# Performance work log

Measured on AMD Instinct MI355X. Metric: run time of the kernel, lower is better.

## Reference

```python
import jax, jax.numpy as jnp
import numpy as np

OUT, IN = 4096, 4096          # weight_shape
T, K, GROUP = 256, 2, 256     # trellis window, bits/weight, weight_scales_group_size
GRID = np.array([-3.0, -1.0, 1.0, 3.0], dtype=np.float32) / np.sqrt(5.0)  # 2-bit symmetric, unit-power


def fwht(x):
    """Normalized fast Walsh-Hadamard transform along the last axis (H = H^T, orthonormal)."""
    n = x.shape[-1]
    orig = x.shape
    y = x.reshape(-1, n)
    rows = y.shape[0]
    h = 1
    while h < n:
        y = y.reshape(rows, n // (2 * h), 2, h)
        a, b = y[:, :, 0, :], y[:, :, 1, :]
        y = jnp.stack([a + b, a - b], axis=2)
        h *= 2
    return y.reshape(orig) * (1.0 / np.sqrt(n)).astype(np.float32)


def fake_quant_u8_per_channel(x):
    """InputQuantizer: 8-bit PER_CHANNEL asymmetric fake-quant over the last (in-channel) dim."""
    red = tuple(range(x.ndim - 1))
    xmin = jnp.min(x, axis=red)
    xmax = jnp.max(x, axis=red)
    scale = jnp.maximum((xmax - xmin) / 255.0, 1e-8)
    zero = jnp.round(-xmin / scale)
    q = jnp.clip(jnp.round(x / scale) + zero, 0.0, 255.0)
    dq = (q - zero) * scale
    # straight-through estimator (matches torch fake-quant training behavior)
    return x + jax.lax.stop_gradient(dq - x)


def decode_trellis(trellis):
    """LowBitSym decode: unpack K=2-bit codes from packed 16-bit trellis words and map
    to the symmetric unit-power 2-bit grid. trellis: (NV, T//16*K) int -> (OUT, IN) float."""
    shifts = jnp.arange(14, -1, -2, dtype=jnp.int32)         # MSB-first 2-bit fields
    codes = (trellis[:, :, None] >> shifts) & 3               # (NV, 32, 8)
    grid = jnp.asarray(GRID)
    return grid[codes].reshape(OUT, IN)


def setup_inputs() -> dict:
    key = jax.random.key(0)
    k1, k2, k3, k4, k5 = jax.random.split(key, 5)
    x = jax.random.normal(k1, (4, 2048, IN), dtype=jnp.float32)
    SU = jax.random.normal(k2, (IN,), dtype=jnp.float32)
    SV = jax.random.normal(k3, (OUT,), dtype=jnp.float32)
    weight_scales = jax.random.uniform(k4, (OUT * IN // GROUP, 1), dtype=jnp.float32)
    trellis = jax.random.randint(k5, (OUT * IN // T, T // 16 * K), 0, 65536, dtype=jnp.int32)
    return {"x": x, "SU": SU, "SV": SV, "weight_scales": weight_scales, "trellis": trellis}


def reference(x, SU, SV, weight_scales, trellis):
    # activation path: incoherence rotate + 8-bit fake quant
    xh = fwht(x * SU)                       # matmul_hadUt_cuda(x * SU)
    xq = fake_quant_u8_per_channel(xh)
    # weight path: trellis decode + Hadamard + SV + grouped scales
    w = decode_trellis(trellis)             # (OUT, IN)
    w = (fwht(w.T) * SV).T                  # (matmul_hadU_cuda(w.T) * SV).T
    w = (w.reshape(-1, GROUP) * weight_scales).reshape(OUT, IN)
    # F.linear(input=xq, weight=w)
    return jnp.einsum('bsi,oi->bso', xq, w)
```

## Files before the change

### kernel.cpp

```cpp
#include <hip/hip_runtime.h>
#include <hip/hip_bf16.h>
#include <stdint.h>

#define IN_DIM 4096
#define OUT_DIM 4096
#define M_ROWS 8192

typedef __attribute__((ext_vector_type(8))) short s16x8;
typedef __attribute__((ext_vector_type(4))) float f32x4;

__device__ __forceinline__ unsigned short f2bf(float f) {
  uint32_t u = __float_as_uint(f);
  uint32_t r = (u + 0x7fffu + ((u >> 16) & 1u)) >> 16;
  return (unsigned short)r;
}
__device__ __forceinline__ float b2f(unsigned short u) {
  return __uint_as_float((uint32_t)u << 16);
}

__device__ __forceinline__ void async16(void* lds, const void* g) {
  __builtin_amdgcn_global_load_lds(
      (const __attribute__((address_space(1))) unsigned int*)g,
      (__attribute__((address_space(3))) unsigned int*)lds, 16, 0, 0);
}

#define FENCE asm volatile("" ::: "memory")

__device__ __forceinline__ void h16(float (&v)[16]) {
#pragma unroll
  for (int h = 1; h < 16; h <<= 1) {
#pragma unroll
    for (int g = 0; g < 8; ++g) {
      int r = g & (h - 1);
      int i0 = ((g & ~(h - 1)) << 1) | r;
      float a = v[i0], b = v[i0 + h];
      v[i0] = a + b;
      v[i0 + h] = a - b;
    }
  }
}

__global__ void fwht_x_kernel(const float* __restrict__ x, const float* __restrict__ SU,
                              unsigned short* __restrict__ xh) {
  __shared__ float s[4352];
  const int row = blockIdx.x;
  const int t = threadIdx.x;
  float v[16];
  const float* xr = x + (size_t)row * IN_DIM;
#pragma unroll
  for (int a = 0; a < 16; ++a) {
    int i = a * 256 + t;
    v[a] = xr[i] * SU[i];
  }
  h16(v);
#pragma unroll
  for (int a = 0; a < 16; ++a) {
    int i = a * 256 + t;
    s[i + (i >> 4)] = v[a];
  }
  __syncthreads();
  const int A = t >> 4, C = t & 15;
#pragma unroll
  for (int b = 0; b < 16; ++b) {
    int i = A * 256 + b * 16 + C;
    v[b] = s[i + (i >> 4)];
  }
  h16(v);
  __syncthreads();
#pragma unroll
  for (int b = 0; b < 16; ++b) {
    int i = A * 256 + b * 16 + C;
    s[i + (i >> 4)] = v[b];
  }
  __syncthreads();
#pragma unroll
  for (int c = 0; c < 16; ++c) {
    int i = t * 16 + c;
    v[c] = s[i + (i >> 4)];
  }
  h16(v);
  unsigned short ob[16];
#pragma unroll
  for (int c = 0; c < 16; ++c) ob[c] = f2bf(v[c] * 0.015625f);
  s16x8* dst = (s16x8*)(xh + (size_t)row * IN_DIM + t * 16);
  dst[0] = *(s16x8*)&ob[0];
  dst[1] = *(s16x8*)&ob[8];
}

__global__ void minmax_part_kernel(const unsigned short* __restrict__ xh,
                                   float* __restrict__ pmin, float* __restrict__ pmax) {
  const int rc = blockIdx.x >> 3;
  const int cb = blockIdx.x & 7;
  const int ch0 = cb * 512 + threadIdx.x * 2;
  float mn0 = 3.4e38f, mx0 = -3.4e38f, mn1 = 3.4e38f, mx1 = -3.4e38f;
  const unsigned int* base =
      (const unsigned int*)(xh + (size_t)rc * 256 * IN_DIM + ch0);
  for (int r = 0; r < 256; ++r) {
    unsigned int u = base[(size_t)r * (IN_DIM / 2)];
    float v0 = __uint_as_float(u << 16);
    float v1 = __uint_as_float(u & 0xffff0000u);
    mn0 = fminf(mn0, v0); mx0 = fmaxf(mx0, v0);
    mn1 = fminf(mn1, v1); mx1 = fmaxf(mx1, v1);
  }
  pmin[rc * IN_DIM + ch0] = mn0;
  pmin[rc * IN_DIM + ch0 + 1] = mn1;
  pmax[rc * IN_DIM + ch0] = mx0;
  pmax[rc * IN_DIM + ch0 + 1] = mx1;
}

__global__ void minmax_fin_kernel(const float* __restrict__ pmin, const float* __restrict__ pmax,
                                  float* __restrict__ scale, float* __restrict__ zero) {
  int ch = blockIdx.x * 256 + threadIdx.x;
  float mn = 3.4e38f, mx = -3.4e38f;
  for (int rc = 0; rc < 32; ++rc) {
    mn = fminf(mn, pmin[rc * IN_DIM + ch]);
    mx = fmaxf(mx, pmax[rc * IN_DIM + ch]);
  }
  float sc = fmaxf((mx - mn) / 255.0f, 1e-8f);
  float zp = rintf(-mn / sc);
  scale[ch] = sc;
  zero[ch] = zp;
}

__global__ void quant_kernel(const unsigned short* __restrict__ xh,
                             const float* __restrict__ scale, const float* __restrict__ zero,
                             unsigned short* __restrict__ xq) {
  const int total8 = M_ROWS * IN_DIM / 8;
  for (int i8 = blockIdx.x * blockDim.x + threadIdx.x; i8 < total8;
       i8 += gridDim.x * blockDim.x) {
    int c8 = i8 & (IN_DIM / 8 - 1);
    s16x8 v = ((const s16x8*)xh)[i8];
    unsigned short o[8];
#pragma unroll
    for (int j = 0; j < 8; ++j) {
      float sc = scale[c8 * 8 + j];
      float zp = zero[c8 * 8 + j];
      float f = b2f((unsigned short)v[j]);
      float q = fminf(fmaxf(rintf(f / sc) + zp, 0.f), 255.f);
      o[j] = f2bf((q - zp) * sc);
    }
    ((s16x8*)xq)[i8] = *(s16x8*)&o[0];
  }
}

#define W_RADIX4(TARR)                                                     \
  for (int h = 1; h < 64; h <<= 2) {                                       \
    __syncthreads();                                                       \
    _Pragma("unroll") for (int j = 0; j < 4; ++j) {                        \
      int g = j * 256 + tid;                                               \
      int c = g & 63, u = g >> 6;                                          \
      int r = u & (h - 1);                                                 \
      int i0 = ((u & ~(h - 1)) << 2) | r;                                  \
      float a = TARR[i0][c], b2 = TARR[i0 + h][c];                         \
      float c2 = TARR[i0 + 2 * h][c], d = TARR[i0 + 3 * h][c];             \
      float y0 = a + b2, y1 = a - b2, y2 = c2 + d, y3 = c2 - d;            \
      TARR[i0][c] = y0 + y2;                                               \
      TARR[i0 + h][c] = y1 + y3;                                           \
      TARR[i0 + 2 * h][c] = y0 - y2;                                       \
      TARR[i0 + 3 * h][c] = y1 - y3;                                       \
    }                                                                      \
  }                                                                        \
  __syncthreads();

__global__ void fwht_w_inner_fused(const int* __restrict__ trellis,
                                   unsigned short* __restrict__ w) {
  __shared__ float t[64][65];
  const int ohi = blockIdx.x >> 6;
  const int it  = blockIdx.x & 63;
  const int tid = threadIdx.x;
  const float g = 0.44721359549995793f;
#pragma unroll
  for (int j = 0; j < 2; ++j) {
    int wi = j * 256 + tid;
    int r = wi >> 3, wc = wi & 7;
    int word = trellis[(size_t)(ohi * 64 + r) * 512 + it * 8 + wc];
#pragma unroll
    for (int jj = 0; jj < 8; ++jj) {
      int code = (word >> (14 - 2 * jj)) & 3;
      t[r][wc * 8 + jj] = (float)(2 * code - 3) * g;
    }
  }
  W_RADIX4(t)
#pragma unroll
  for (int j = 0; j < 16; ++j) {
    int e = j * 256 + tid;
    int r = e >> 6, c = e & 63;
    w[((size_t)(ohi * 64 + r)) * IN_DIM + it * 64 + c] = f2bf(t[r][c]);
  }
}

__global__ void fwht_w_outer(const unsigned short* __restrict__ w,
                             const float* __restrict__ SV,
                             const float* __restrict__ wscale, unsigned short* __restrict__ wq) {
  __shared__ float t[64][65];
  const int olo = blockIdx.x >> 6;
  const int it  = blockIdx.x & 63;
  const int tid = threadIdx.x;
#pragma unroll
  for (int j = 0; j < 16; ++j) {
    int e = j * 256 + tid;
    int r = e >> 6, c = e & 63;
    t[r][c] = b2f(w[((size_t)(r * 64 + olo)) * IN_DIM + it * 64 + c]);
  }
  W_RADIX4(t)
#pragma unroll
  for (int j = 0; j < 16; ++j) {
    int e = j * 256 + tid;
    int r = e >> 6, c = e & 63;
    int o = r * 64 + olo;
    int i = it * 64 + c;
    float val = t[r][c] * 0.015625f * SV[o] * wscale[(o << 4) + (i >> 8)];
    wq[(size_t)o * IN_DIM + i] = f2bf(val);
  }
}

__global__ __launch_bounds__(512, 2) void gemm256_kernel(
    const unsigned short* __restrict__ A, const unsigned short* __restrict__ B,
    float* __restrict__ C) {
  __shared__ __align__(16) unsigned short lds[65536];
  const int tid  = threadIdx.x;
  const int lane = tid & 63;
  const int wave = tid >> 6;
  const int wm = wave >> 2, wn = wave & 3;
  const int fr = lane & 15, kqi = lane >> 4;
  const int swz = fr & 7;

  const int b  = blockIdx.x;
  const int wg = (b & 7) * 64 + (b >> 3);
  const int bm = wg >> 4, bn = wg & 15;
  const int gm0 = bm * 256, gn0 = bn * 256;

  f32x4 acc[2][2][4][2] = {};
  s16x8 af0[4][2], af1[4][2];
  s16x8 bf0[2][2], bf1[2][2];

  const int F0 = tid, F1 = 512 + tid;
  const int rh0 = F0 >> 3, s0 = (F0 & 7) ^ (rh0 & 7);
  const int rh1 = F1 >> 3, s1 = (F1 & 7) ^ (rh1 & 7);
  auto stage = [&](const unsigned short* gbase, int grow0, int kcol, int ldsoff) {
    async16((void*)&lds[ldsoff + F0 * 8],
            (const void*)(gbase + (size_t)(grow0 + rh0) * IN_DIM + kcol + s0 * 8));
    async16((void*)&lds[ldsoff + F1 * 8],
            (const void*)(gbase + (size_t)(grow0 + rh1) * IN_DIM + kcol + s1 * 8));
  };

#define READ_AF2(DST, QM, TBUF, MIH)                                                      \
  {                                                                                       \
    const int abase = (TBUF) * 16384 + (QM) * 8192;                                       \
    _Pragma("unroll") for (int kk = 0; kk < 2; ++kk)                                      \
      _Pragma("unroll") for (int mi = 2 * (MIH); mi < 2 * (MIH) + 2; ++mi) {              \
        int rh = wm * 64 + mi * 16 + fr;                                                  \
        DST[mi][kk] = *(const s16x8*)&lds[abase + rh * 64 + (((kk * 4 + kqi) ^ swz) * 8)];\
      }                                                                                   \
  }
#define READ_BF2(DST, QN, TBUF, NI)                                                       \
  {                                                                                       \
    const int bbase = 32768 + (TBUF) * 16384 + (QN) * 8192;                               \
    const int rh = wn * 32 + (NI) * 16 + fr;                                              \
    _Pragma("unroll") for (int kk = 0; kk < 2; ++kk)                                      \
      DST[NI][kk] = *(const s16x8*)&lds[bbase + rh * 64 + (((kk * 4 + kqi) ^ swz) * 8)];  \
  }
#define MFMA16(QM, QN, AF, BF)                                                            \
    _Pragma("unroll") for (int kk = 0; kk < 2; ++kk)                                      \
      _Pragma("unroll") for (int mi = 0; mi < 4; ++mi)                                    \
        _Pragma("unroll") for (int ni = 0; ni < 2; ++ni)                                  \
          acc[QM][QN][mi][ni] = __builtin_amdgcn_mfma_f32_16x16x32_bf16(                  \
              AF[mi][kk], BF[ni][kk], acc[QM][QN][mi][ni], 0, 0, 0);
#define PHASE_BEGIN(SGBASE, SGROW0, SKCOL, SLDSOFF, VM)                                   \
    stage(SGBASE, SGROW0, SKCOL, SLDSOFF);                                                \
    FENCE;                                                                                \
    asm volatile("s_waitcnt vmcnt(" #VM ")" ::: "memory");                                \
    __builtin_amdgcn_s_barrier();                                                         \
    FENCE;                                                                                \
    __builtin_amdgcn_s_setprio(1);
#define PHASE_END                                                                         \
    __builtin_amdgcn_s_setprio(0);                                                        \
    FENCE;                                                                                \
    __builtin_amdgcn_s_barrier();                                                         \
    FENCE;

  stage(A, gm0,       0, 0);
  stage(B, gn0,       0, 32768);
  stage(A, gm0 + 128, 0, 8192);
  stage(B, gn0 + 128, 0, 40960);
  stage(A, gm0,      64, 16384);
  stage(B, gn0,      64, 49152);
  FENCE;
  asm volatile("s_waitcnt vmcnt(8)" ::: "memory");
  __builtin_amdgcn_s_barrier();
  FENCE;
  READ_AF2(af0, 0, 0, 0)
  READ_BF2(bf0, 0, 0, 0)

  for (int it = 0; it < 32; ++it) {
    const int k1 = ((2 * it + 1) * 64) & 4095;
    const int k2 = ((2 * it + 2) * 64) & 4095;
    const int k3 = ((2 * it + 3) * 64) & 4095;
    READ_AF2(af0, 0, 0, 1) READ_BF2(bf0, 0, 0, 1)
    PHASE_BEGIN(A, gm0 + 128, k1, 24576, 6)
    MFMA16(0, 0, af0, bf0)
    READ_BF2(bf1, 1, 0, 0) READ_BF2(bf1, 1, 0, 1)
    PHASE_END
    PHASE_BEGIN(B, gn0 + 128, k1, 57344, 63)
    MFMA16(0, 1, af0, bf1)
    READ_AF2(af1, 1, 0, 0)
    PHASE_END
    READ_AF2(af1, 1, 0, 1)
    PHASE_BEGIN(A, gm0,       k2, 0,     63)
    MFMA16(1, 1, af1, bf1)
    PHASE_END
    PHASE_BEGIN(B, gn0,       k2, 32768, 8)
    MFMA16(1, 0, af1, bf0)
    READ_AF2(af0, 0, 1, 0) READ_BF2(bf0, 0, 1, 0)
    PHASE_END
    READ_AF2(af0, 0, 1, 1) READ_BF2(bf0, 0, 1, 1)
    PHASE_BEGIN(A, gm0 + 128, k2, 8192,  6)
    MFMA16(0, 0, af0, bf0)
    READ_BF2(bf1, 1, 1, 0) READ_BF2(bf1, 1, 1, 1)
    PHASE_END
    PHASE_BEGIN(B, gn0 + 128, k2, 40960, 63)
    MFMA16(0, 1, af0, bf1)
    READ_AF2(af1, 1, 1, 0)
    PHASE_END
    READ_AF2(af1, 1, 1, 1)
    PHASE_BEGIN(A, gm0,       k3, 16384, 63)
    MFMA16(1, 1, af1, bf1)
    PHASE_END
    PHASE_BEGIN(B, gn0,       k3, 49152, 8)
    MFMA16(1, 0, af1, bf0)
    READ_AF2(af0, 0, 0, 0) READ_BF2(bf0, 0, 0, 0)
    PHASE_END
  }
#undef PHASE_BEGIN
#undef PHASE_END
#undef MFMA16
#undef READ_AF2
#undef READ_BF2
  asm volatile("s_waitcnt vmcnt(0)" ::: "memory");

  const int orow = kqi * 4;
#pragma unroll
  for (int qm = 0; qm < 2; ++qm)
#pragma unroll
    for (int qn = 0; qn < 2; ++qn)
#pragma unroll
      for (int mi = 0; mi < 4; ++mi)
#pragma unroll
        for (int ni = 0; ni < 2; ++ni) {
          const int row0 = gm0 + qm * 128 + wm * 64 + mi * 16 + orow;
          const int col  = gn0 + qn * 128 + wn * 32 + ni * 16 + fr;
          f32x4 v = acc[qm][qn][mi][ni];
#pragma unroll
          for (int r = 0; r < 4; ++r)
            C[(size_t)(row0 + r) * OUT_DIM + col] = v[r];
        }
}

extern "C" void kernel_launch(void* const* d_in, const int* in_sizes, int n_in,
                              void* d_out, int out_size, void* d_ws, size_t ws_size,
                              hipStream_t stream) {
  const float* x      = (const float*)d_in[0];
  const float* SU     = (const float*)d_in[1];
  const float* SV     = (const float*)d_in[2];
  const float* wscale = (const float*)d_in[3];
  const int* trellis  = (const int*)d_in[4];
  float* out = (float*)d_out;

  char* ws = (char*)d_ws;
  unsigned short* xq = (unsigned short*)ws;
  unsigned short* wq = (unsigned short*)(ws + (size_t)67108864);
  float* pmin  = (float*)(ws + (size_t)67108864);
  float* pmax  = (float*)(ws + (size_t)67108864 + 524288);
  float* scale = (float*)(ws + (size_t)67108864 + 1048576);
  float* zero  = (float*)(ws + (size_t)67108864 + 1064960);

  unsigned short* xh   = (unsigned short*)out;
  unsigned short* wdec = (unsigned short*)out + (size_t)33554432;

  hipLaunchKernelGGL(fwht_x_kernel, dim3(M_ROWS), dim3(256), 0, stream, x, SU, xh);
  hipLaunchKernelGGL(minmax_part_kernel, dim3(256), dim3(256), 0, stream, xh, pmin, pmax);
  hipLaunchKernelGGL(minmax_fin_kernel, dim3(16), dim3(256), 0, stream, pmin, pmax, scale, zero);
  hipLaunchKernelGGL(quant_kernel, dim3(2048), dim3(256), 0, stream, xh, scale, zero, xq);
  hipLaunchKernelGGL(fwht_w_inner_fused, dim3(4096), dim3(256), 0, stream, trellis, wdec);
  hipLaunchKernelGGL(fwht_w_outer, dim3(4096), dim3(256), 0, stream, wdec, SV, wscale, wq);
  hipLaunchKernelGGL(gemm256_kernel, dim3((M_ROWS / 256) * (OUT_DIM / 256)), dim3(512), 0,
                     stream, xq, wq, out);
}
```

Baseline: 336.2 us.

## Fuse weight FWHT into one kernel and merge min/max finalize via atomics

New measurement: 357.6 us. 1.06x slower.

```diff
diff --git a/kernel.cpp b/kernel.cpp
--- a/kernel.cpp
+++ b/kernel.cpp
@@ -16,6 +16,14 @@
 }
 __device__ __forceinline__ float b2f(unsigned short u) {
   return __uint_as_float((uint32_t)u << 16);
+}
+__device__ __forceinline__ unsigned int fmap(float f) {
+  unsigned int u = __float_as_uint(f);
+  return ((int)u >= 0) ? (u | 0x80000000u) : ~u;
+}
+__device__ __forceinline__ float funmap(unsigned int u) {
+  unsigned int b = (u & 0x80000000u) ? (u & 0x7fffffffu) : ~u;
+  return __uint_as_float(b);
 }
 
 __device__ __forceinline__ void async16(void* lds, const void* g) {
@@ -88,7 +96,8 @@
 }
 
 __global__ void minmax_part_kernel(const unsigned short* __restrict__ xh,
-                                   float* __restrict__ pmin, float* __restrict__ pmax) {
+                                   unsigned int* __restrict__ gminU,
+                                   unsigned int* __restrict__ gmaxU) {
   const int rc = blockIdx.x >> 3;
   const int cb = blockIdx.x & 7;
   const int ch0 = cb * 512 + threadIdx.x * 2;
@@ -102,28 +111,15 @@
     mn0 = fminf(mn0, v0); mx0 = fmaxf(mx0, v0);
     mn1 = fminf(mn1, v1); mx1 = fmaxf(mx1, v1);
   }
-  pmin[rc * IN_DIM + ch0] = mn0;
-  pmin[rc * IN_DIM + ch0 + 1] = mn1;
-  pmax[rc * IN_DIM + ch0] = mx0;
-  pmax[rc * IN_DIM + ch0 + 1] = mx1;
-}
-
-__global__ void minmax_fin_kernel(const float* __restrict__ pmin, const float* __restrict__ pmax,
-                                  float* __restrict__ scale, float* __restrict__ zero) {
-  int ch = blockIdx.x * 256 + threadIdx.x;
-  float mn = 3.4e38f, mx = -3.4e38f;
-  for (int rc = 0; rc < 32; ++rc) {
-    mn = fminf(mn, pmin[rc * IN_DIM + ch]);
-    mx = fmaxf(mx, pmax[rc * IN_DIM + ch]);
-  }
-  float sc = fmaxf((mx - mn) / 255.0f, 1e-8f);
-  float zp = rintf(-mn / sc);
-  scale[ch] = sc;
-  zero[ch] = zp;
+  atomicMin(&gminU[ch0], fmap(mn0));
+  atomicMin(&gminU[ch0 + 1], fmap(mn1));
+  atomicMax(&gmaxU[ch0], fmap(mx0));
+  atomicMax(&gmaxU[ch0 + 1], fmap(mx1));
 }
 
 __global__ void quant_kernel(const unsigned short* __restrict__ xh,
-                             const float* __restrict__ scale, const float* __restrict__ zero,
+                             const unsigned int* __restrict__ gminU,
+                             const unsigned int* __restrict__ gmaxU,
                              unsigned short* __restrict__ xq) {
   const int total8 = M_ROWS * IN_DIM / 8;
   for (int i8 = blockIdx.x * blockDim.x + threadIdx.x; i8 < total8;
@@ -133,8 +129,10 @@
     unsigned short o[8];
 #pragma unroll
     for (int j = 0; j < 8; ++j) {
-      float sc = scale[c8 * 8 + j];
-      float zp = zero[c8 * 8 + j];
+      float mn = funmap(gminU[c8 * 8 + j]);
+      float mx = funmap(gmaxU[c8 * 8 + j]);
+      float sc = fmaxf((mx - mn) * (1.0f / 255.0f), 1e-8f);
+      float zp = rintf(-mn / sc);
       float f = b2f((unsigned short)v[j]);
       float q = fminf(fmaxf(rintf(f / sc) + zp, 0.f), 255.f);
       o[j] = f2bf((q - zp) * sc);
@@ -143,74 +141,78 @@
   }
 }
 
-#define W_RADIX4(TARR)                                                     \
-  for (int h = 1; h < 64; h <<= 2) {                                       \
-    __syncthreads();                                                       \
-    _Pragma("unroll") for (int j = 0; j < 4; ++j) {                        \
-      int g = j * 256 + tid;                                               \
-      int c = g & 63, u = g >> 6;                                          \
-      int r = u & (h - 1);                                                 \
-      int i0 = ((u & ~(h - 1)) << 2) | r;                                  \
-      float a = TARR[i0][c], b2 = TARR[i0 + h][c];                         \
-      float c2 = TARR[i0 + 2 * h][c], d = TARR[i0 + 3 * h][c];             \
-      float y0 = a + b2, y1 = a - b2, y2 = c2 + d, y3 = c2 - d;            \
-      TARR[i0][c] = y0 + y2;                                               \
-      TARR[i0 + h][c] = y1 + y3;                                           \
-      TARR[i0 + 2 * h][c] = y0 - y2;                                       \
-      TARR[i0 + 3 * h][c] = y1 - y3;                                       \
-    }                                                                      \
-  }                                                                        \
-  __syncthreads();
-
-__global__ void fwht_w_inner_fused(const int* __restrict__ trellis,
-                                   unsigned short* __restrict__ w) {
-  __shared__ float t[64][65];
-  const int ohi = blockIdx.x >> 6;
-  const int it  = blockIdx.x & 63;
+#define PADA(idx) ((idx) + ((idx) >> 5))
+__global__ __launch_bounds__(1024) void fwht_w_fused(const int* __restrict__ trellis,
+                                                     const float* __restrict__ SV,
+                                                     const float* __restrict__ wscale,
+                                                     unsigned short* __restrict__ wq) {
+  __shared__ float t[16896];
+  const int b = blockIdx.x;
+  const int w = (b & 7) * 128 + (b >> 3);
+  const int ib = w >> 1;
+  const int half = w & 1;
   const int tid = threadIdx.x;
   const float g = 0.44721359549995793f;
-#pragma unroll
-  for (int j = 0; j < 2; ++j) {
-    int wi = j * 256 + tid;
-    int r = wi >> 3, wc = wi & 7;
-    int word = trellis[(size_t)(ohi * 64 + r) * 512 + it * 8 + wc];
-#pragma unroll
-    for (int jj = 0; jj < 8; ++jj) {
-      int code = (word >> (14 - 2 * jj)) & 3;
-      t[r][wc * 8 + jj] = (float)(2 * code - 3) * g;
+
+#pragma unroll
+  for (int j = 0; j < 4; ++j) {
+    int o = j * 1024 + tid;
+    int word = trellis[(size_t)o * 512 + ib];
+#pragma unroll
+    for (int dl = 0; dl < 4; ++dl) {
+      int d = half * 4 + dl;
+      int code = (word >> (14 - 2 * d)) & 3;
+      int idx = dl * 4096 + o;
+      t[PADA(idx)] = (float)(2 * code - 3) * g;
     }
   }
-  W_RADIX4(t)
-#pragma unroll
-  for (int j = 0; j < 16; ++j) {
-    int e = j * 256 + tid;
-    int r = e >> 6, c = e & 63;
-    w[((size_t)(ohi * 64 + r)) * IN_DIM + it * 64 + c] = f2bf(t[r][c]);
-  }
-}
-
-__global__ void fwht_w_outer(const unsigned short* __restrict__ w,
-                             const float* __restrict__ SV,
-                             const float* __restrict__ wscale, unsigned short* __restrict__ wq) {
-  __shared__ float t[64][65];
-  const int olo = blockIdx.x >> 6;
-  const int it  = blockIdx.x & 63;
-  const int tid = threadIdx.x;
-#pragma unroll
-  for (int j = 0; j < 16; ++j) {
-    int e = j * 256 + tid;
-    int r = e >> 6, c = e & 63;
-    t[r][c] = b2f(w[((size_t)(r * 64 + olo)) * IN_DIM + it * 64 + c]);
-  }
-  W_RADIX4(t)
-#pragma unroll
-  for (int j = 0; j < 16; ++j) {
-    int e = j * 256 + tid;
-    int r = e >> 6, c = e & 63;
-    int o = r * 64 + olo;
-    int i = it * 64 + c;
-    float val = t[r][c] * 0.015625f * SV[o] * wscale[(o << 4) + (i >> 8)];
-    wq[(size_t)o * IN_DIM + i] = f2bf(val);
+  __syncthreads();
+
+  float v[16];
+  {
+    const int dl = tid >> 8, u = tid & 255;
+    const int base = dl * 4096 + u * 16;
+#pragma unroll
+    for (int lo = 0; lo < 16; ++lo) v[lo] = t[PADA(base + lo)];
+    h16(v);
+    __syncthreads();
+#pragma unroll
+    for (int lo = 0; lo < 16; ++lo) t[PADA(base + lo)] = v[lo];
+  }
+  __syncthreads();
+  {
+    const int dl = tid >> 8, hi = (tid >> 4) & 15, lo = tid & 15;
+    const int base = dl * 4096 + hi * 256 + lo;
+#pragma unroll
+    for (int m = 0; m < 16; ++m) v[m] = t[PADA(base + m * 16)];
+    h16(v);
+    __syncthreads();
+#pragma unroll
+    for (int m = 0; m < 16; ++m) t[PADA(base + m * 16)] = v[m];
+  }
+  __syncthreads();
+  {
+    const int dl = tid >> 8, m = (tid >> 4) & 15, lo = tid & 15;
+    const int base = dl * 4096 + m * 16 + lo;
+#pragma unroll
+    for (int k = 0; k < 16; ++k) v[k] = t[PADA(base + k * 256)];
+    h16(v);
+    __syncthreads();
+#pragma unroll
+    for (int k = 0; k < 16; ++k) t[PADA(base + k * 256)] = v[k];
+  }
+  __syncthreads();
+
+  const int wsc_col = ib >> 5;
+#pragma unroll
+  for (int j = 0; j < 4; ++j) {
+    int o = j * 1024 + tid;
+    float sv = SV[o] * 0.015625f * wscale[(o << 4) + wsc_col];
+    unsigned short ob[4];
+#pragma unroll
+    for (int dl = 0; dl < 4; ++dl)
+      ob[dl] = f2bf(t[PADA(dl * 4096 + o)] * sv);
+    *(uint2*)(wq + ((size_t)ib << 15) + o * 8 + half * 4) = *(uint2*)&ob[0];
   }
 }
 
@@ -237,11 +239,18 @@
   const int F0 = tid, F1 = 512 + tid;
   const int rh0 = F0 >> 3, s0 = (F0 & 7) ^ (rh0 & 7);
   const int rh1 = F1 >> 3, s1 = (F1 & 7) ^ (rh1 & 7);
-  auto stage = [&](const unsigned short* gbase, int grow0, int kcol, int ldsoff) {
+  auto stageA = [&](int grow0, int kcol, int ldsoff) {
     async16((void*)&lds[ldsoff + F0 * 8],
-            (const void*)(gbase + (size_t)(grow0 + rh0) * IN_DIM + kcol + s0 * 8));
+            (const void*)(A + (size_t)(grow0 + rh0) * IN_DIM + kcol + s0 * 8));
     async16((void*)&lds[ldsoff + F1 * 8],
-            (const void*)(gbase + (size_t)(grow0 + rh1) * IN_DIM + kcol + s1 * 8));
+            (const void*)(A + (size_t)(grow0 + rh1) * IN_DIM + kcol + s1 * 8));
+  };
+  auto stageB = [&](int grow0, int kcol, int ldsoff) {
+    const int sg0 = kcol >> 3;
+    async16((void*)&lds[ldsoff + F0 * 8],
+            (const void*)(B + (((size_t)(sg0 + s0)) << 15) + (grow0 + rh0) * 8));
+    async16((void*)&lds[ldsoff + F1 * 8],
+            (const void*)(B + (((size_t)(sg0 + s1)) << 15) + (grow0 + rh1) * 8));
   };
 
 #define READ_AF2(DST, QM, TBUF, MIH)                                                      \
@@ -266,8 +275,15 @@
         _Pragma("unroll") for (int ni = 0; ni < 2; ++ni)                                  \
           acc[QM][QN][mi][ni] = __builtin_amdgcn_mfma_f32_16x16x32_bf16(                  \
               AF[mi][kk], BF[ni][kk], acc[QM][QN][mi][ni], 0, 0, 0);
-#define PHASE_BEGIN(SGBASE, SGROW0, SKCOL, SLDSOFF, VM)                                   \
-    stage(SGBASE, SGROW0, SKCOL, SLDSOFF);                                                \
+#define PHASE_BEGIN_A(SGROW0, SKCOL, SLDSOFF, VM)                                         \
+    stageA(SGROW0, SKCOL, SLDSOFF);                                                       \
+    FENCE;                                                                                \
+    asm volatile("s_waitcnt vmcnt(" #VM ")" ::: "memory");                                \
+    __builtin_amdgcn_s_barrier();                                                         \
+    FENCE;                                                                                \
+    __builtin_amdgcn_s_setprio(1);
+#define PHASE_BEGIN_B(SGROW0, SKCOL, SLDSOFF, VM)                                         \
+    stageB(SGROW0, SKCOL, SLDSOFF);                                                       \
     FENCE;                                                                                \
     asm volatile("s_waitcnt vmcnt(" #VM ")" ::: "memory");                                \
     __builtin_amdgcn_s_barrier();                                                         \
@@ -279,12 +295,12 @@
     __builtin_amdgcn_s_barrier();                                                         \
     FENCE;
 
-  stage(A, gm0,       0, 0);
-  stage(B, gn0,       0, 32768);
-  stage(A, gm0 + 128, 0, 8192);
-  stage(B, gn0 + 128, 0, 40960);
-  stage(A, gm0,      64, 16384);
-  stage(B, gn0,      64, 49152);
+  stageA(gm0,       0, 0);
+  stageB(gn0,       0, 32768);
+  stageA(gm0 + 128, 0, 8192);
+  stageB(gn0 + 128, 0, 40960);
+  stageA(gm0,      64, 16384);
+  stageB(gn0,      64, 49152);
   FENCE;
   asm volatile("s_waitcnt vmcnt(8)" ::: "memory");
   __builtin_amdgcn_s_barrier();
@@ -297,41 +313,42 @@
     const int k2 = ((2 * it + 2) * 64) & 4095;
     const int k3 = ((2 * it + 3) * 64) & 4095;
     READ_AF2(af0, 0, 0, 1) READ_BF2(bf0, 0, 0, 1)
-    PHASE_BEGIN(A, gm0 + 128, k1, 24576, 6)
+    PHASE_BEGIN_A(gm0 + 128, k1, 24576, 6)
     MFMA16(0, 0, af0, bf0)
     READ_BF2(bf1, 1, 0, 0) READ_BF2(bf1, 1, 0, 1)
     PHASE_END
-    PHASE_BEGIN(B, gn0 + 128, k1, 57344, 63)
+    PHASE_BEGIN_B(gn0 + 128, k1, 57344, 63)
     MFMA16(0, 1, af0, bf1)
     READ_AF2(af1, 1, 0, 0)
     PHASE_END
     READ_AF2(af1, 1, 0, 1)
-    PHASE_BEGIN(A, gm0,       k2, 0,     63)
+    PHASE_BEGIN_A(gm0,       k2, 0,     63)
     MFMA16(1, 1, af1, bf1)
     PHASE_END
-    PHASE_BEGIN(B, gn0,       k2, 32768, 8)
+    PHASE_BEGIN_B(gn0,       k2, 32768, 8)
     MFMA16(1, 0, af1, bf0)
     READ_AF2(af0, 0, 1, 0) READ_BF2(bf0, 0, 1, 0)
     PHASE_END
     READ_AF2(af0, 0, 1, 1) READ_BF2(bf0, 0, 1, 1)
-    PHASE_BEGIN(A, gm0 + 128, k2, 8192,  6)
+    PHASE_BEGIN_A(gm0 + 128, k2, 8192,  6)
     MFMA16(0, 0, af0, bf0)
     READ_BF2(bf1, 1, 1, 0) READ_BF2(bf1, 1, 1, 1)
     PHASE_END
-    PHASE_BEGIN(B, gn0 + 128, k2, 40960, 63)
+    PHASE_BEGIN_B(gn0 + 128, k2, 40960, 63)
     MFMA16(0, 1, af0, bf1)
     READ_AF2(af1, 1, 1, 0)
     PHASE_END
     READ_AF2(af1, 1, 1, 1)
-    PHASE_BEGIN(A, gm0,       k3, 16384, 63)
+    PHASE_BEGIN_A(gm0,       k3, 16384, 63)
     MFMA16(1, 1, af1, bf1)
     PHASE_END
-    PHASE_BEGIN(B, gn0,       k3, 49152, 8)
+    PHASE_BEGIN_B(gn0,       k3, 49152, 8)
     MFMA16(1, 0, af1, bf0)
     READ_AF2(af0, 0, 0, 0) READ_BF2(bf0, 0, 0, 0)
     PHASE_END
   }
-#undef PHASE_BEGIN
+#undef PHASE_BEGIN_A
+#undef PHASE_BEGIN_B
 #undef PHASE_END
 #undef MFMA16
 #undef READ_AF2
@@ -369,20 +386,17 @@
   char* ws = (char*)d_ws;
   unsigned short* xq = (unsigned short*)ws;
   unsigned short* wq = (unsigned short*)(ws + (size_t)67108864);
-  float* pmin  = (float*)(ws + (size_t)67108864);
-  float* pmax  = (float*)(ws + (size_t)67108864 + 524288);
-  float* scale = (float*)(ws + (size_t)67108864 + 1048576);
-  float* zero  = (float*)(ws + (size_t)67108864 + 1064960);
-
-  unsigned short* xh   = (unsigned short*)out;
-  unsigned short* wdec = (unsigned short*)out + (size_t)33554432;
-
+  unsigned int* gminU = (unsigned int*)(ws + (size_t)67108864);
+  unsigned int* gmaxU = (unsigned int*)(ws + (size_t)67108864 + 16384);
+
+  unsigned short* xh = (unsigned short*)out;
+
+  hipMemsetAsync(gminU, 0xFF, 16384, stream);
+  hipMemsetAsync(gmaxU, 0x00, 16384, stream);
   hipLaunchKernelGGL(fwht_x_kernel, dim3(M_ROWS), dim3(256), 0, stream, x, SU, xh);
-  hipLaunchKernelGGL(minmax_part_kernel, dim3(256), dim3(256), 0, stream, xh, pmin, pmax);
-  hipLaunchKernelGGL(minmax_fin_kernel, dim3(16), dim3(256), 0, stream, pmin, pmax, scale, zero);
-  hipLaunchKernelGGL(quant_kernel, dim3(2048), dim3(256), 0, stream, xh, scale, zero, xq);
-  hipLaunchKernelGGL(fwht_w_inner_fused, dim3(4096), dim3(256), 0, stream, trellis, wdec);
-  hipLaunchKernelGGL(fwht_w_outer, dim3(4096), dim3(256), 0, stream, wdec, SV, wscale, wq);
+  hipLaunchKernelGGL(minmax_part_kernel, dim3(256), dim3(256), 0, stream, xh, gminU, gmaxU);
+  hipLaunchKernelGGL(quant_kernel, dim3(2048), dim3(256), 0, stream, xh, gminU, gmaxU, xq);
+  hipLaunchKernelGGL(fwht_w_fused, dim3(1024), dim3(1024), 0, stream, trellis, SV, wscale, wq);
   hipLaunchKernelGGL(gemm256_kernel, dim3((M_ROWS / 256) * (OUT_DIM / 256)), dim3(512), 0,
                      stream, xq, wq, out);
 }
```

## Fuse per-channel min/max partials into x Hadamard kernel with multi-row blocks

Applied to the files above, without the earlier changes.

After: 345.8 us. 2.8% more time.

```diff
diff --git a/kernel.cpp b/kernel.cpp
--- a/kernel.cpp
+++ b/kernel.cpp
@@ -40,81 +40,88 @@
   }
 }
 
-__global__ void fwht_x_kernel(const float* __restrict__ x, const float* __restrict__ SU,
-                              unsigned short* __restrict__ xh) {
+__global__ __launch_bounds__(256) void fwht_x_kernel(
+    const float* __restrict__ x, const float* __restrict__ SU,
+    unsigned short* __restrict__ xh,
+    float* __restrict__ pmin, float* __restrict__ pmax) {
   __shared__ float s[4352];
-  const int row = blockIdx.x;
   const int t = threadIdx.x;
-  float v[16];
-  const float* xr = x + (size_t)row * IN_DIM;
-#pragma unroll
-  for (int a = 0; a < 16; ++a) {
-    int i = a * 256 + t;
-    v[a] = xr[i] * SU[i];
-  }
-  h16(v);
-#pragma unroll
-  for (int a = 0; a < 16; ++a) {
-    int i = a * 256 + t;
-    s[i + (i >> 4)] = v[a];
-  }
-  __syncthreads();
-  const int A = t >> 4, C = t & 15;
-#pragma unroll
-  for (int b = 0; b < 16; ++b) {
-    int i = A * 256 + b * 16 + C;
-    v[b] = s[i + (i >> 4)];
-  }
-  h16(v);
-  __syncthreads();
-#pragma unroll
-  for (int b = 0; b < 16; ++b) {
-    int i = A * 256 + b * 16 + C;
-    s[i + (i >> 4)] = v[b];
-  }
-  __syncthreads();
-#pragma unroll
-  for (int c = 0; c < 16; ++c) {
-    int i = t * 16 + c;
-    v[c] = s[i + (i >> 4)];
-  }
-  h16(v);
-  unsigned short ob[16];
-#pragma unroll
-  for (int c = 0; c < 16; ++c) ob[c] = f2bf(v[c] * 0.015625f);
-  s16x8* dst = (s16x8*)(xh + (size_t)row * IN_DIM + t * 16);
-  dst[0] = *(s16x8*)&ob[0];
-  dst[1] = *(s16x8*)&ob[8];
-}
-
-__global__ void minmax_part_kernel(const unsigned short* __restrict__ xh,
-                                   float* __restrict__ pmin, float* __restrict__ pmax) {
-  const int rc = blockIdx.x >> 3;
-  const int cb = blockIdx.x & 7;
-  const int ch0 = cb * 512 + threadIdx.x * 2;
-  float mn0 = 3.4e38f, mx0 = -3.4e38f, mn1 = 3.4e38f, mx1 = -3.4e38f;
-  const unsigned int* base =
-      (const unsigned int*)(xh + (size_t)rc * 256 * IN_DIM + ch0);
-  for (int r = 0; r < 256; ++r) {
-    unsigned int u = base[(size_t)r * (IN_DIM / 2)];
-    float v0 = __uint_as_float(u << 16);
-    float v1 = __uint_as_float(u & 0xffff0000u);
-    mn0 = fminf(mn0, v0); mx0 = fmaxf(mx0, v0);
-    mn1 = fminf(mn1, v1); mx1 = fmaxf(mx1, v1);
-  }
-  pmin[rc * IN_DIM + ch0] = mn0;
-  pmin[rc * IN_DIM + ch0 + 1] = mn1;
-  pmax[rc * IN_DIM + ch0] = mx0;
-  pmax[rc * IN_DIM + ch0 + 1] = mx1;
+  const int row0 = blockIdx.x * 16;
+  float su[16];
+#pragma unroll
+  for (int a = 0; a < 16; ++a) su[a] = SU[a * 256 + t];
+  float mn[16], mx[16];
+#pragma unroll
+  for (int c = 0; c < 16; ++c) { mn[c] = 3.4e38f; mx[c] = -3.4e38f; }
+  float xv[16];
+#pragma unroll
+  for (int a = 0; a < 16; ++a) xv[a] = x[(size_t)row0 * IN_DIM + a * 256 + t];
+
+  for (int rr = 0; rr < 16; ++rr) {
+    float v[16];
+#pragma unroll
+    for (int a = 0; a < 16; ++a) v[a] = xv[a] * su[a];
+    if (rr < 15) {
+      const float* xr = x + (size_t)(row0 + rr + 1) * IN_DIM;
+#pragma unroll
+      for (int a = 0; a < 16; ++a) xv[a] = xr[a * 256 + t];
+    }
+    h16(v);
+    __syncthreads();
+#pragma unroll
+    for (int a = 0; a < 16; ++a) {
+      int i = a * 256 + t;
+      s[i + (i >> 4)] = v[a];
+    }
+    __syncthreads();
+    const int A = t >> 4, C = t & 15;
+#pragma unroll
+    for (int b = 0; b < 16; ++b) {
+      int i = A * 256 + b * 16 + C;
+      v[b] = s[i + (i >> 4)];
+    }
+    h16(v);
+    __syncthreads();
+#pragma unroll
+    for (int b = 0; b < 16; ++b) {
+      int i = A * 256 + b * 16 + C;
+      s[i + (i >> 4)] = v[b];
+    }
+    __syncthreads();
+#pragma unroll
+    for (int c = 0; c < 16; ++c) {
+      int i = t * 16 + c;
+      v[c] = s[i + (i >> 4)];
+    }
+    h16(v);
+    unsigned short ob[16];
+#pragma unroll
+    for (int c = 0; c < 16; ++c) {
+      ob[c] = f2bf(v[c] * 0.015625f);
+      float bv = b2f(ob[c]);
+      mn[c] = fminf(mn[c], bv);
+      mx[c] = fmaxf(mx[c], bv);
+    }
+    s16x8* dst = (s16x8*)(xh + (size_t)(row0 + rr) * IN_DIM + t * 16);
+    dst[0] = *(s16x8*)&ob[0];
+    dst[1] = *(s16x8*)&ob[8];
+  }
+  float4* pm = (float4*)(pmin + (size_t)blockIdx.x * IN_DIM + t * 16);
+  float4* px = (float4*)(pmax + (size_t)blockIdx.x * IN_DIM + t * 16);
+#pragma unroll
+  for (int q = 0; q < 4; ++q) {
+    pm[q] = *(float4*)&mn[q * 4];
+    px[q] = *(float4*)&mx[q * 4];
+  }
 }
 
 __global__ void minmax_fin_kernel(const float* __restrict__ pmin, const float* __restrict__ pmax,
                                   float* __restrict__ scale, float* __restrict__ zero) {
   int ch = blockIdx.x * 256 + threadIdx.x;
   float mn = 3.4e38f, mx = -3.4e38f;
-  for (int rc = 0; rc < 32; ++rc) {
-    mn = fminf(mn, pmin[rc * IN_DIM + ch]);
-    mx = fmaxf(mx, pmax[rc * IN_DIM + ch]);
+  for (int rc = 0; rc < 512; ++rc) {
+    mn = fminf(mn, pmin[(size_t)rc * IN_DIM + ch]);
+    mx = fmaxf(mx, pmax[(size_t)rc * IN_DIM + ch]);
   }
   float sc = fmaxf((mx - mn) / 255.0f, 1e-8f);
   float zp = rintf(-mn / sc);
@@ -370,15 +377,14 @@
   unsigned short* xq = (unsigned short*)ws;
   unsigned short* wq = (unsigned short*)(ws + (size_t)67108864);
   float* pmin  = (float*)(ws + (size_t)67108864);
-  float* pmax  = (float*)(ws + (size_t)67108864 + 524288);
-  float* scale = (float*)(ws + (size_t)67108864 + 1048576);
-  float* zero  = (float*)(ws + (size_t)67108864 + 1064960);
+  float* pmax  = (float*)(ws + (size_t)67108864 + 8388608);
+  float* scale = (float*)(ws + (size_t)67108864 + 16777216);
+  float* zero  = (float*)(ws + (size_t)67108864 + 16793600);
 
   unsigned short* xh   = (unsigned short*)out;
   unsigned short* wdec = (unsigned short*)out + (size_t)33554432;
 
-  hipLaunchKernelGGL(fwht_x_kernel, dim3(M_ROWS), dim3(256), 0, stream, x, SU, xh);
-  hipLaunchKernelGGL(minmax_part_kernel, dim3(256), dim3(256), 0, stream, xh, pmin, pmax);
+  hipLaunchKernelGGL(fwht_x_kernel, dim3(512), dim3(256), 0, stream, x, SU, xh, pmin, pmax);
   hipLaunchKernelGGL(minmax_fin_kernel, dim3(16), dim3(256), 0, stream, pmin, pmax, scale, zero);
   hipLaunchKernelGGL(quant_kernel, dim3(2048), dim3(256), 0, stream, xh, scale, zero, xq);
   hipLaunchKernelGGL(fwht_w_inner_fused, dim3(4096), dim3(256), 0, stream, trellis, wdec);
```

## Merge activation and weight preprocessing kernels into combined block-dispatched launches

Applied to the files above, without the earlier changes.

After: 328.1 us. 2.4% less time.

```diff
diff --git a/kernel.cpp b/kernel.cpp
--- a/kernel.cpp
+++ b/kernel.cpp
@@ -40,115 +40,12 @@
   }
 }
 
-__global__ void fwht_x_kernel(const float* __restrict__ x, const float* __restrict__ SU,
-                              unsigned short* __restrict__ xh) {
-  __shared__ float s[4352];
-  const int row = blockIdx.x;
-  const int t = threadIdx.x;
-  float v[16];
-  const float* xr = x + (size_t)row * IN_DIM;
-#pragma unroll
-  for (int a = 0; a < 16; ++a) {
-    int i = a * 256 + t;
-    v[a] = xr[i] * SU[i];
-  }
-  h16(v);
-#pragma unroll
-  for (int a = 0; a < 16; ++a) {
-    int i = a * 256 + t;
-    s[i + (i >> 4)] = v[a];
-  }
-  __syncthreads();
-  const int A = t >> 4, C = t & 15;
-#pragma unroll
-  for (int b = 0; b < 16; ++b) {
-    int i = A * 256 + b * 16 + C;
-    v[b] = s[i + (i >> 4)];
-  }
-  h16(v);
-  __syncthreads();
-#pragma unroll
-  for (int b = 0; b < 16; ++b) {
-    int i = A * 256 + b * 16 + C;
-    s[i + (i >> 4)] = v[b];
-  }
-  __syncthreads();
-#pragma unroll
-  for (int c = 0; c < 16; ++c) {
-    int i = t * 16 + c;
-    v[c] = s[i + (i >> 4)];
-  }
-  h16(v);
-  unsigned short ob[16];
-#pragma unroll
-  for (int c = 0; c < 16; ++c) ob[c] = f2bf(v[c] * 0.015625f);
-  s16x8* dst = (s16x8*)(xh + (size_t)row * IN_DIM + t * 16);
-  dst[0] = *(s16x8*)&ob[0];
-  dst[1] = *(s16x8*)&ob[8];
-}
-
-__global__ void minmax_part_kernel(const unsigned short* __restrict__ xh,
-                                   float* __restrict__ pmin, float* __restrict__ pmax) {
-  const int rc = blockIdx.x >> 3;
-  const int cb = blockIdx.x & 7;
-  const int ch0 = cb * 512 + threadIdx.x * 2;
-  float mn0 = 3.4e38f, mx0 = -3.4e38f, mn1 = 3.4e38f, mx1 = -3.4e38f;
-  const unsigned int* base =
-      (const unsigned int*)(xh + (size_t)rc * 256 * IN_DIM + ch0);
-  for (int r = 0; r < 256; ++r) {
-    unsigned int u = base[(size_t)r * (IN_DIM / 2)];
-    float v0 = __uint_as_float(u << 16);
-    float v1 = __uint_as_float(u & 0xffff0000u);
-    mn0 = fminf(mn0, v0); mx0 = fmaxf(mx0, v0);
-    mn1 = fminf(mn1, v1); mx1 = fmaxf(mx1, v1);
-  }
-  pmin[rc * IN_DIM + ch0] = mn0;
-  pmin[rc * IN_DIM + ch0 + 1] = mn1;
-  pmax[rc * IN_DIM + ch0] = mx0;
-  pmax[rc * IN_DIM + ch0 + 1] = mx1;
-}
-
-__global__ void minmax_fin_kernel(const float* __restrict__ pmin, const float* __restrict__ pmax,
-                                  float* __restrict__ scale, float* __restrict__ zero) {
-  int ch = blockIdx.x * 256 + threadIdx.x;
-  float mn = 3.4e38f, mx = -3.4e38f;
-  for (int rc = 0; rc < 32; ++rc) {
-    mn = fminf(mn, pmin[rc * IN_DIM + ch]);
-    mx = fmaxf(mx, pmax[rc * IN_DIM + ch]);
-  }
-  float sc = fmaxf((mx - mn) / 255.0f, 1e-8f);
-  float zp = rintf(-mn / sc);
-  scale[ch] = sc;
-  zero[ch] = zp;
-}
-
-__global__ void quant_kernel(const unsigned short* __restrict__ xh,
-                             const float* __restrict__ scale, const float* __restrict__ zero,
-                             unsigned short* __restrict__ xq) {
-  const int total8 = M_ROWS * IN_DIM / 8;
-  for (int i8 = blockIdx.x * blockDim.x + threadIdx.x; i8 < total8;
-       i8 += gridDim.x * blockDim.x) {
-    int c8 = i8 & (IN_DIM / 8 - 1);
-    s16x8 v = ((const s16x8*)xh)[i8];
-    unsigned short o[8];
-#pragma unroll
-    for (int j = 0; j < 8; ++j) {
-      float sc = scale[c8 * 8 + j];
-      float zp = zero[c8 * 8 + j];
-      float f = b2f((unsigned short)v[j]);
-      float q = fminf(fmaxf(rintf(f / sc) + zp, 0.f), 255.f);
-      o[j] = f2bf((q - zp) * sc);
-    }
-    ((s16x8*)xq)[i8] = *(s16x8*)&o[0];
-  }
-}
-
 #define W_RADIX4(TARR)                                                     \
   for (int h = 1; h < 64; h <<= 2) {                                       \
     __syncthreads();                                                       \
     _Pragma("unroll") for (int j = 0; j < 4; ++j) {                        \
-      int g = j * 256 + tid;                                               \
-      int c = g & 63, u = g >> 6;                                          \
+      int g2 = j * 256 + tid;                                              \
+      int c = g2 & 63, u = g2 >> 6;                                        \
       int r = u & (h - 1);                                                 \
       int i0 = ((u & ~(h - 1)) << 2) | r;                                  \
       float a = TARR[i0][c], b2 = TARR[i0 + h][c];                         \
@@ -162,55 +59,164 @@
   }                                                                        \
   __syncthreads();
 
-__global__ void fwht_w_inner_fused(const int* __restrict__ trellis,
-                                   unsigned short* __restrict__ w) {
-  __shared__ float t[64][65];
-  const int ohi = blockIdx.x >> 6;
-  const int it  = blockIdx.x & 63;
+__global__ __launch_bounds__(256) void pre1_kernel(
+    const float* __restrict__ x, const float* __restrict__ SU,
+    unsigned short* __restrict__ xh,
+    const int* __restrict__ trellis, unsigned short* __restrict__ wdec) {
+  __shared__ __align__(16) char smem[17408];
   const int tid = threadIdx.x;
-  const float g = 0.44721359549995793f;
-#pragma unroll
-  for (int j = 0; j < 2; ++j) {
-    int wi = j * 256 + tid;
-    int r = wi >> 3, wc = wi & 7;
-    int word = trellis[(size_t)(ohi * 64 + r) * 512 + it * 8 + wc];
-#pragma unroll
-    for (int jj = 0; jj < 8; ++jj) {
-      int code = (word >> (14 - 2 * jj)) & 3;
-      t[r][wc * 8 + jj] = (float)(2 * code - 3) * g;
-    }
-  }
-  W_RADIX4(t)
-#pragma unroll
-  for (int j = 0; j < 16; ++j) {
-    int e = j * 256 + tid;
-    int r = e >> 6, c = e & 63;
-    w[((size_t)(ohi * 64 + r)) * IN_DIM + it * 64 + c] = f2bf(t[r][c]);
-  }
-}
-
-__global__ void fwht_w_outer(const unsigned short* __restrict__ w,
-                             const float* __restrict__ SV,
-                             const float* __restrict__ wscale, unsigned short* __restrict__ wq) {
-  __shared__ float t[64][65];
-  const int olo = blockIdx.x >> 6;
-  const int it  = blockIdx.x & 63;
+  if (blockIdx.x < 8192) {
+    float* s = (float*)smem;
+    const int row = blockIdx.x;
+    const int t = tid;
+    float v[16];
+    const float* xr = x + (size_t)row * IN_DIM;
+#pragma unroll
+    for (int a = 0; a < 16; ++a) {
+      int i = a * 256 + t;
+      v[a] = xr[i] * SU[i];
+    }
+    h16(v);
+#pragma unroll
+    for (int a = 0; a < 16; ++a) {
+      int i = a * 256 + t;
+      s[i + (i >> 4)] = v[a];
+    }
+    __syncthreads();
+    const int A = t >> 4, C = t & 15;
+#pragma unroll
+    for (int b = 0; b < 16; ++b) {
+      int i = A * 256 + b * 16 + C;
+      v[b] = s[i + (i >> 4)];
+    }
+    h16(v);
+    __syncthreads();
+#pragma unroll
+    for (int b = 0; b < 16; ++b) {
+      int i = A * 256 + b * 16 + C;
+      s[i + (i >> 4)] = v[b];
+    }
+    __syncthreads();
+#pragma unroll
+    for (int c = 0; c < 16; ++c) {
+      int i = t * 16 + c;
+      v[c] = s[i + (i >> 4)];
+    }
+    h16(v);
+    unsigned short ob[16];
+#pragma unroll
+    for (int c = 0; c < 16; ++c) ob[c] = f2bf(v[c] * 0.015625f);
+    s16x8* dst = (s16x8*)(xh + (size_t)row * IN_DIM + t * 16);
+    dst[0] = *(s16x8*)&ob[0];
+    dst[1] = *(s16x8*)&ob[8];
+  } else {
+    float (*t)[65] = (float(*)[65])smem;
+    const int b = blockIdx.x - 8192;
+    const int ohi = b >> 6;
+    const int it  = b & 63;
+    const float g = 0.44721359549995793f;
+#pragma unroll
+    for (int j = 0; j < 2; ++j) {
+      int wi = j * 256 + tid;
+      int r = wi >> 3, wc = wi & 7;
+      int word = trellis[(size_t)(ohi * 64 + r) * 512 + it * 8 + wc];
+#pragma unroll
+      for (int jj = 0; jj < 8; ++jj) {
+        int code = (word >> (14 - 2 * jj)) & 3;
+        t[r][wc * 8 + jj] = (float)(2 * code - 3) * g;
+      }
+    }
+    W_RADIX4(t)
+#pragma unroll
+    for (int j = 0; j < 16; ++j) {
+      int e = j * 256 + tid;
+      int r = e >> 6, c = e & 63;
+      wdec[((size_t)(ohi * 64 + r)) * IN_DIM + it * 64 + c] = f2bf(t[r][c]);
+    }
+  }
+}
+
+__global__ __launch_bounds__(256) void pre2_kernel(
+    const unsigned short* __restrict__ xh,
+    float* __restrict__ pmin, float* __restrict__ pmax,
+    const unsigned short* __restrict__ wdec, const float* __restrict__ SV,
+    const float* __restrict__ wscale, unsigned short* __restrict__ wq) {
+  __shared__ __align__(16) char smem[16640];
   const int tid = threadIdx.x;
-#pragma unroll
-  for (int j = 0; j < 16; ++j) {
-    int e = j * 256 + tid;
-    int r = e >> 6, c = e & 63;
-    t[r][c] = b2f(w[((size_t)(r * 64 + olo)) * IN_DIM + it * 64 + c]);
-  }
-  W_RADIX4(t)
-#pragma unroll
-  for (int j = 0; j < 16; ++j) {
-    int e = j * 256 + tid;
-    int r = e >> 6, c = e & 63;
-    int o = r * 64 + olo;
-    int i = it * 64 + c;
-    float val = t[r][c] * 0.015625f * SV[o] * wscale[(o << 4) + (i >> 8)];
-    wq[(size_t)o * IN_DIM + i] = f2bf(val);
+  if (blockIdx.x < 256) {
+    const int rc = blockIdx.x >> 3;
+    const int cb = blockIdx.x & 7;
+    const int ch0 = cb * 512 + tid * 2;
+    float mn0 = 3.4e38f, mx0 = -3.4e38f, mn1 = 3.4e38f, mx1 = -3.4e38f;
+    const unsigned int* base =
+        (const unsigned int*)(xh + (size_t)rc * 256 * IN_DIM + ch0);
+    for (int r = 0; r < 256; ++r) {
+      unsigned int u = base[(size_t)r * (IN_DIM / 2)];
+      float v0 = __uint_as_float(u << 16);
+      float v1 = __uint_as_float(u & 0xffff0000u);
+      mn0 = fminf(mn0, v0); mx0 = fmaxf(mx0, v0);
+      mn1 = fminf(mn1, v1); mx1 = fmaxf(mx1, v1);
+    }
+    pmin[rc * IN_DIM + ch0] = mn0;
+    pmin[rc * IN_DIM + ch0 + 1] = mn1;
+    pmax[rc * IN_DIM + ch0] = mx0;
+    pmax[rc * IN_DIM + ch0 + 1] = mx1;
+  } else {
+    float (*t)[65] = (float(*)[65])smem;
+    const int b = blockIdx.x - 256;
+    const int olo = b >> 6;
+    const int it  = b & 63;
+#pragma unroll
+    for (int j = 0; j < 16; ++j) {
+      int e = j * 256 + tid;
+      int r = e >> 6, c = e & 63;
+      t[r][c] = b2f(wdec[((size_t)(r * 64 + olo)) * IN_DIM + it * 64 + c]);
+    }
+    W_RADIX4(t)
+#pragma unroll
+    for (int j = 0; j < 16; ++j) {
+      int e = j * 256 + tid;
+      int r = e >> 6, c = e & 63;
+      int o = r * 64 + olo;
+      int i = it * 64 + c;
+      float val = t[r][c] * 0.015625f * SV[o] * wscale[(o << 4) + (i >> 8)];
+      wq[(size_t)o * IN_DIM + i] = f2bf(val);
+    }
+  }
+}
+
+__global__ void minmax_fin_kernel(const float* __restrict__ pmin, const float* __restrict__ pmax,
+                                  float* __restrict__ scale, float* __restrict__ zero) {
+  int ch = blockIdx.x * 256 + threadIdx.x;
+  float mn = 3.4e38f, mx = -3.4e38f;
+  for (int rc = 0; rc < 32; ++rc) {
+    mn = fminf(mn, pmin[rc * IN_DIM + ch]);
+    mx = fmaxf(mx, pmax[rc * IN_DIM + ch]);
+  }
+  float sc = fmaxf((mx - mn) / 255.0f, 1e-8f);
+  float zp = rintf(-mn / sc);
+  scale[ch] = sc;
+  zero[ch] = zp;
+}
+
+__global__ void quant_kernel(const unsigned short* __restrict__ xh,
+                             const float* __restrict__ scale, const float* __restrict__ zero,
+                             unsigned short* __restrict__ xq) {
+  const int total8 = M_ROWS * IN_DIM / 8;
+  for (int i8 = blockIdx.x * blockDim.x + threadIdx.x; i8 < total8;
+       i8 += gridDim.x * blockDim.x) {
+    int c8 = i8 & (IN_DIM / 8 - 1);
+    s16x8 v = ((const s16x8*)xh)[i8];
+    unsigned short o[8];
+#pragma unroll
+    for (int j = 0; j < 8; ++j) {
+      float sc = scale[c8 * 8 + j];
+      float zp = zero[c8 * 8 + j];
+      float f = b2f((unsigned short)v[j]);
+      float q = fminf(fmaxf(rintf(f / sc) + zp, 0.f), 255.f);
+      o[j] = f2bf((q - zp) * sc);
+    }
+    ((s16x8*)xq)[i8] = *(s16x8*)&o[0];
   }
 }
 
@@ -369,20 +375,22 @@
   char* ws = (char*)d_ws;
   unsigned short* xq = (unsigned short*)ws;
   unsigned short* wq = (unsigned short*)(ws + (size_t)67108864);
-  float* pmin  = (float*)(ws + (size_t)67108864);
-  float* pmax  = (float*)(ws + (size_t)67108864 + 524288);
-  float* scale = (float*)(ws + (size_t)67108864 + 1048576);
-  float* zero  = (float*)(ws + (size_t)67108864 + 1064960);
 
   unsigned short* xh   = (unsigned short*)out;
   unsigned short* wdec = (unsigned short*)out + (size_t)33554432;
-
-  hipLaunchKernelGGL(fwht_x_kernel, dim3(M_ROWS), dim3(256), 0, stream, x, SU, xh);
-  hipLaunchKernelGGL(minmax_part_kernel, dim3(256), dim3(256), 0, stream, xh, pmin, pmax);
-  hipLaunchKernelGGL(minmax_fin_kernel, dim3(16), dim3(256), 0, stream, pmin, pmax, scale, zero);
+  char* outb = (char*)out;
+  float* pmin  = (float*)(outb + (size_t)100663296);
+  float* pmax  = (float*)(outb + (size_t)100663296 + 524288);
+  float* scale = (float*)(outb + (size_t)100663296 + 1048576);
+  float* zero  = (float*)(outb + (size_t)100663296 + 1064960);
+
+  hipLaunchKernelGGL(pre1_kernel, dim3(12288), dim3(256), 0, stream,
+                     x, SU, xh, trellis, wdec);
+  hipLaunchKernelGGL(pre2_kernel, dim3(4352), dim3(256), 0, stream,
+                     xh, pmin, pmax, wdec, SV, wscale, wq);
+  hipLaunchKernelGGL(minmax_fin_kernel, dim3(16), dim3(256), 0, stream,
+                     pmin, pmax, scale, zero);
   hipLaunchKernelGGL(quant_kernel, dim3(2048), dim3(256), 0, stream, xh, scale, zero, xq);
-  hipLaunchKernelGGL(fwht_w_inner_fused, dim3(4096), dim3(256), 0, stream, trellis, wdec);
-  hipLaunchKernelGGL(fwht_w_outer, dim3(4096), dim3(256), 0, stream, wdec, SV, wscale, wq);
   hipLaunchKernelGGL(gemm256_kernel, dim3((M_ROWS / 256) * (OUT_DIM / 256)), dim3(512), 0,
                      stream, xq, wq, out);
 }
```
